# Kernel tuning notes

Measured on AMD Instinct MI355X. Metric: run time of the kernel, lower is better.

## Reference

```python
import jax, jax.numpy as jnp
import numpy as np

BETA = 0.95
THRESH = 1.0
T = 25
MAXD = 11      # dilated_kernel_size: 250//25=10 -> bumped to odd 11
LP = 10        # left_pad = 250//25
B = 1024
SIGINIT = 5.0  # max_delay // 2, SIG is frozen at this value


@jax.custom_vjp
def atan_spike(u):
    # heaviside forward, atan surrogate gradient (snntorch surrogate.atan, alpha=2)
    return (u > 0).astype(u.dtype)

def _atan_fwd(u):
    return atan_spike(u), u

def _atan_bwd(u, g):
    return (g / (1.0 + (jnp.pi * u) ** 2),)

atan_spike.defvjp(_atan_fwd, _atan_bwd)


def dcls_kernel(W, P, SIG):
    # DCLS 'gauss': gaussian-interpolated dense kernel.
    # W: (O, I, kc), P/SIG: (1, O, I, kc) -> dense kernel (O, I, MAXD)
    idx = jnp.arange(MAXD, dtype=W.dtype)
    Pc = P[0] + MAXD // 2                      # center positions in dense kernel
    S = jnp.abs(SIG[0]) + 0.27                 # sigma floor (DCLS epsilon)
    X = jnp.exp(-0.5 * ((idx[:, None, None, None] - Pc) / S) ** 2)  # (K,O,I,kc)
    X = X / (X.sum(axis=0, keepdims=True) + 1e-7)
    return jnp.einsum('oic,joic->oij', W, X)


def dcls_conv(x, W, P, SIG, b):
    # x: (B, C_in, L) -> (B, C_out, L - MAXD + 1), VALID conv like padding=0
    k = dcls_kernel(W, P, SIG)
    y = jax.lax.conv_general_dilated(x, k, (1,), 'VALID',
                                     dimension_numbers=('NCH', 'OIH', 'NCH'))
    return y + b[None, :, None]


def batchnorm(x, gamma, beta, mean, var, eps=1e-5):
    # eval-mode BatchNorm1d over (B, C, L)
    inv = gamma / jnp.sqrt(var + eps)
    return (x - mean[None, :, None]) * inv[None, :, None] + beta[None, :, None]


def lif_scan(x):
    # snntorch Leaky, reset_mechanism='subtract'; x: (B, C, T) input currents
    xT = jnp.moveaxis(x, 2, 0)  # (T, B, C)

    def step(mem, xt):
        reset = jax.lax.stop_gradient(atan_spike(mem - THRESH))  # detached reset
        mem = BETA * mem + xt - reset * THRESH
        spk = atan_spike(mem - THRESH)
        return mem, (spk, mem)

    _, (spk, mem) = jax.lax.scan(step, jnp.zeros_like(xT[0]), xT)
    return spk, mem  # each (T, B, C)


def pad_left(x):
    return jnp.pad(x, ((0, 0), (0, 0), (LP, 0)))


def setup_inputs() -> dict:
    key = jax.random.key(0)
    ks = jax.random.split(key, 16)

    def w_init(k, o, i):
        return jax.random.normal(k, (o, i, 1), jnp.float32) / np.sqrt(i)

    inp = {
        'data': jax.random.normal(ks[0], (B, T, 140), jnp.float32),
        'W1': w_init(ks[1], 256, 140),
        'b1': jax.random.normal(ks[2], (256,), jnp.float32) * 0.01,
        'P1': jax.random.uniform(ks[3], (1, 256, 140, 1), jnp.float32, -SIGINIT, SIGINIT),
        'SIG1': jnp.full((1, 256, 140, 1), SIGINIT, jnp.float32),
        'bn1_gamma': jax.random.uniform(ks[4], (256,), jnp.float32, 0.5, 1.5),
        'bn1_beta': jax.random.normal(ks[5], (256,), jnp.float32) * 0.1,
        'bn1_mean': jax.random.normal(ks[6], (256,), jnp.float32) * 0.1,
        'bn1_var': jax.random.uniform(ks[7], (256,), jnp.float32, 0.5, 1.5),
        'W2': w_init(ks[8], 256, 256),
        'b2': jax.random.normal(ks[9], (256,), jnp.float32) * 0.01,
        'P2': jax.random.uniform(ks[10], (1, 256, 256, 1), jnp.float32, -SIGINIT, SIGINIT),
        'SIG2': jnp.full((1, 256, 256, 1), SIGINIT, jnp.float32),
        'bn2_gamma': jax.random.uniform(ks[11], (256,), jnp.float32, 0.5, 1.5),
        'bn2_beta': jax.random.normal(ks[12], (256,), jnp.float32) * 0.1,
        'bn2_mean': jax.random.normal(ks[13], (256,), jnp.float32) * 0.1,
        'bn2_var': jax.random.uniform(ks[14], (256,), jnp.float32, 0.5, 1.5),
        'W3': w_init(ks[15], 20, 256),
        'b3': jnp.zeros((20,), jnp.float32),
        'P3': jax.random.uniform(jax.random.fold_in(key, 99), (1, 20, 256, 1), jnp.float32, -SIGINIT, SIGINIT),
        'SIG3': jnp.full((1, 20, 256, 1), SIGINIT, jnp.float32),
    }
    return inp


def reference(data, W1, b1, P1, SIG1, bn1_gamma, bn1_beta, bn1_mean, bn1_var,
              W2, b2, P2, SIG2, bn2_gamma, bn2_beta, bn2_mean, bn2_var,
              W3, b3, P3, SIG3):
    # data: (B, T, 140); pad time dim on the left, then to (B, C, L)
    x = jnp.moveaxis(jnp.pad(data, ((0, 0), (LP, 0), (0, 0))), 1, 2)  # (B,140,T+LP)
    x = batchnorm(dcls_conv(x, W1, P1, SIG1, b1), bn1_gamma, bn1_beta, bn1_mean, bn1_var)
    spk1, _ = lif_scan(x)                  # (T, B, 256)
    in1 = jnp.moveaxis(spk1, 0, 2)         # (B, 256, T)  (dropout eval = identity)

    x = batchnorm(dcls_conv(pad_left(in1), W2, P2, SIG2, b2),
                  bn2_gamma, bn2_beta, bn2_mean, bn2_var)
    spk2, _ = lif_scan(x)
    in2 = jnp.moveaxis(spk2, 0, 2)         # (B, 256, T)

    x = dcls_conv(pad_left(in2), W3, P3, SIG3, b3)  # (B, 20, T)
    spk3, mem3 = lif_scan(x)               # (T, B, 20) each
    return spk3, mem3
```

## Files before the change

### kernel.cpp

```cpp
#include <hip/hip_runtime.h>
#include <math.h>

#define BB 1024
#define TT 25
#define LP 10
#define MAXD 11

#define XR2 26
#define XC 264
#define XSZ2 (XR2 * XC)

#define IC1 140
#define ICP1 160
#define XC1 168
#define XSZ1 (XR2 * XC1)
#define SS1 (2 * XSZ1)

typedef __bf16 bf16x8 __attribute__((ext_vector_type(8)));
typedef float  f32x4  __attribute__((ext_vector_type(4)));

#define MFMA16(A, B, C) __builtin_amdgcn_mfma_f32_16x16x32_bf16((A), (B), (C), 0, 0, 0)

__global__ void gen_trip(const float* __restrict__ W,
                         const float* __restrict__ P,
                         const float* __restrict__ SIG,
                         __bf16* __restrict__ Khi, __bf16* __restrict__ Kmid,
                         __bf16* __restrict__ Klo,
                         int O, int Opad, int I, int Ipad) {
    int idx = blockIdx.x * blockDim.x + threadIdx.x;
    if (idx >= Opad * Ipad) return;
    int i = idx % Ipad;
    int o = idx / Ipad;
    if (o >= O || i >= I) {
#pragma unroll
        for (int j = 0; j < MAXD; ++j) {
            size_t ofs = ((size_t)(j * Opad + o)) * Ipad + i;
            Khi[ofs] = (__bf16)0.0f;
            Kmid[ofs] = (__bf16)0.0f;
            Klo[ofs] = (__bf16)0.0f;
        }
        return;
    }
    int widx = o * I + i;
    float w  = W[widx];
    float pc = P[widx] + (float)(MAXD / 2);
    float s  = fabsf(SIG[widx]) + 0.27f;
    float x[MAXD];
    float sum = 0.f;
#pragma unroll
    for (int j = 0; j < MAXD; ++j) {
        float d = ((float)j - pc) / s;
        x[j] = expf(-0.5f * d * d);
        sum += x[j];
    }
    float denom = sum + 1e-7f;
#pragma unroll
    for (int j = 0; j < MAXD; ++j) {
        float kv = w * (x[j] / denom);
        __bf16 h = (__bf16)kv;
        float  r1 = kv - (float)h;
        __bf16 m = (__bf16)r1;
        float  r2 = r1 - (float)m;
        __bf16 l = (__bf16)r2;
        size_t ofs = ((size_t)(j * Opad + o)) * Ipad + i;
        Khi[ofs] = h;
        Kmid[ofs] = m;
        Klo[ofs] = l;
    }
}

__global__ __launch_bounds__(512, 2)
void conv1_mfma(const float* __restrict__ xin,
                const __bf16* __restrict__ Khi,
                const __bf16* __restrict__ Kmid,
                const __bf16* __restrict__ Klo,
                const float* __restrict__ bias,
                const float* __restrict__ gamma,
                const float* __restrict__ beta,
                const float* __restrict__ mean,
                const float* __restrict__ var,
                __bf16* __restrict__ spk1) {
    __shared__ __align__(16) char smem[3 * SS1 * 2];
    __bf16* xs = (__bf16*)smem;
    float*  ys = (float*)smem;

    const int rr = blockIdx.x & 7;
    const int gg = blockIdx.x >> 3;
    const int pp = 2 * (rr + 8 * (gg >> 1)) + (gg & 1);
    const int b0 = pp * 2;

    const int tid  = threadIdx.x;
    const int w    = tid >> 6;
    const int lane = tid & 63;
    const int lm   = lane & 15;
    const int quad = lane >> 4;

    {
        uint32_t* xz = (uint32_t*)smem;
        for (int k = tid; k < 3 * SS1 / 2; k += 512) xz[k] = 0u;
    }
    __syncthreads();
#pragma unroll
    for (int bl = 0; bl < 2; ++bl) {
        const float* src = xin + (size_t)(b0 + bl) * (TT * IC1);
        for (int k = tid; k < TT * IC1; k += 512) {
            int t = k / IC1;
            int i = k - t * IC1;
            float x  = src[k];
            __bf16 h = (__bf16)x;
            float r1 = x - (float)h;
            __bf16 m = (__bf16)r1;
            float r2 = r1 - (float)m;
            __bf16 l = (__bf16)r2;
            int ofs = bl * XSZ1 + t * XC1 + i;
            xs[0 * SS1 + ofs] = h;
            xs[1 * SS1 + ofs] = m;
            xs[2 * SS1 + ofs] = l;
        }
    }
    __syncthreads();

    f32x4 acc[2][4];
#pragma unroll
    for (int p = 0; p < 2; ++p)
#pragma unroll
        for (int nt = 0; nt < 4; ++nt) acc[p][nt] = (f32x4){0.f, 0.f, 0.f, 0.f};

    auto loadA = [&](int n, bf16x8* Ah, bf16x8* Am, bf16x8* Al) {
        n = (n > 54) ? 54 : n;
        const int j = n / 5;
        const int ic = n - 5 * j;
        const size_t base =
            (size_t)(j * 256 + w * 32 + lm) * ICP1 + ic * 32 + quad * 8;
#pragma unroll
        for (int p = 0; p < 2; ++p) {
            Ah[p] = *(const bf16x8*)(Khi  + base + p * 16 * ICP1);
            Am[p] = *(const bf16x8*)(Kmid + base + p * 16 * ICP1);
            Al[p] = *(const bf16x8*)(Klo  + base + p * 16 * ICP1);
        }
    };

    auto step = [&](int n, bf16x8* Ah, bf16x8* Am, bf16x8* Al) {
        const int j = n / 5;
        const int ic = n - 5 * j;
        int r0 = lm + j - 10;          r0 = ((unsigned)r0 < 25u) ? r0 : 25;
        int r1 = 16 + lm + j - 10;     r1 = ((unsigned)r1 < 25u) ? r1 : 25;
        const int col = ic * 32 + quad * 8;
#pragma unroll
        for (int bl = 0; bl < 2; ++bl) {
            bf16x8 Bh[2], Bm[2], Bl[2];
#pragma unroll
            for (int th = 0; th < 2; ++th) {
                const int row = th ? r1 : r0;
                const int ofs = bl * XSZ1 + row * XC1 + col;
                Bh[th] = *(const bf16x8*)&xs[0 * SS1 + ofs];
                Bm[th] = *(const bf16x8*)&xs[1 * SS1 + ofs];
                Bl[th] = *(const bf16x8*)&xs[2 * SS1 + ofs];
            }
#pragma unroll
            for (int p = 0; p < 2; ++p)
#pragma unroll
                for (int th = 0; th < 2; ++th)
                    acc[p][bl * 2 + th] = MFMA16(Ah[p], Bh[th], acc[p][bl * 2 + th]);
#pragma unroll
            for (int p = 0; p < 2; ++p)
#pragma unroll
                for (int th = 0; th < 2; ++th)
                    acc[p][bl * 2 + th] = MFMA16(Ah[p], Bm[th], acc[p][bl * 2 + th]);
#pragma unroll
            for (int p = 0; p < 2; ++p)
#pragma unroll
                for (int th = 0; th < 2; ++th)
                    acc[p][bl * 2 + th] = MFMA16(Am[p], Bh[th], acc[p][bl * 2 + th]);
#pragma unroll
            for (int p = 0; p < 2; ++p)
#pragma unroll
                for (int th = 0; th < 2; ++th)
                    acc[p][bl * 2 + th] = MFMA16(Ah[p], Bl[th], acc[p][bl * 2 + th]);
#pragma unroll
            for (int p = 0; p < 2; ++p)
#pragma unroll
                for (int th = 0; th < 2; ++th)
                    acc[p][bl * 2 + th] = MFMA16(Am[p], Bm[th], acc[p][bl * 2 + th]);
#pragma unroll
            for (int p = 0; p < 2; ++p)
#pragma unroll
                for (int th = 0; th < 2; ++th)
                    acc[p][bl * 2 + th] = MFMA16(Al[p], Bh[th], acc[p][bl * 2 + th]);
        }
    };

    bf16x8 A0h[2], A0m[2], A0l[2], A1h[2], A1m[2], A1l[2];
    loadA(0, A0h, A0m, A0l);
    for (int n = 0; n < 54; n += 2) {
        loadA(n + 1, A1h, A1m, A1l);
        step(n, A0h, A0m, A0l);
        loadA(n + 2, A0h, A0m, A0l);
        step(n + 1, A1h, A1m, A1l);
    }
    step(54, A0h, A0m, A0l);

#pragma unroll
    for (int bl = 0; bl < 2; ++bl) {
        __syncthreads();
#pragma unroll
        for (int p = 0; p < 2; ++p)
#pragma unroll
            for (int th = 0; th < 2; ++th) {
                int t = th * 16 + lm;
                if (t < TT) {
                    int ob = w * 32 + p * 16 + quad * 4;
#pragma unroll
                    for (int v = 0; v < 4; ++v)
                        ys[(ob + v) * 27 + t] = acc[p][bl * 2 + th][v];
                }
            }
        __syncthreads();
        if (tid < 256) {
            const int o = tid;
            float scale = gamma[o] / sqrtf(var[o] + 1e-5f);
            float ofs   = (bias[o] - mean[o]) * scale + beta[o];
            unsigned short* dst =
                (unsigned short*)spk1 + (size_t)(b0 + bl) * (TT * 256) + o;
            const float* yrow = &ys[o * 27];
            float memv = 0.f;
#pragma unroll
            for (int t = 0; t < TT; ++t) {
                float a     = yrow[t] * scale + ofs;
                float reset = (memv > 1.0f) ? 1.0f : 0.f;
                memv        = 0.95f * memv + a - reset;
                dst[t * 256] = (memv > 1.0f) ? 0x3F80 : 0;
            }
        }
    }
}

__global__ __launch_bounds__(1024, 1)
void conv23_mfma(const __bf16* __restrict__ spk1,
                 const __bf16* __restrict__ Khi,
                 const __bf16* __restrict__ Kmid,
                 const __bf16* __restrict__ Klo,
                 const float* __restrict__ bias,
                 const float* __restrict__ gamma,
                 const float* __restrict__ beta,
                 const float* __restrict__ mean,
                 const float* __restrict__ var,
                 const __bf16* __restrict__ K3hi,
                 const __bf16* __restrict__ K3mid,
                 const __bf16* __restrict__ K3lo,
                 const float* __restrict__ b3,
                 float* __restrict__ out) {
    __shared__ __align__(16) char smem[61568];
    __bf16* xs  = (__bf16*)smem;
    float*  ysq = (float*)(smem + 54912);
    float*  ys3 = (float*)smem;

    const int b0   = blockIdx.x * 4;
    const int tid  = threadIdx.x;
    const int w    = tid >> 6;
    const int lane = tid & 63;
    const int lm   = lane & 15;
    const int quad = lane >> 4;

    for (int k = tid; k < 4 * (XC / 2); k += 1024) {
        int bl = k / (XC / 2);
        int c  = k % (XC / 2);
        ((uint32_t*)xs)[(bl * XSZ2 + 25 * XC) / 2 + c] = 0u;
    }
    for (int k = tid; k < 4 * 800; k += 1024) {
        int bl = k / 800;
        int v  = k % 800;
        int t  = v >> 5;
        int iv = v & 31;
        uint4 d = ((const uint4*)(spk1 + (size_t)(b0 + bl) * (TT * 256)))[v];
        *(uint4*)&xs[bl * XSZ2 + t * XC + iv * 8] = d;
    }
    __syncthreads();

    f32x4 acc[8];
#pragma unroll
    for (int nt = 0; nt < 8; ++nt) acc[nt] = (f32x4){0.f, 0.f, 0.f, 0.f};

    {
        auto loadA = [&](int n, bf16x8* Ah, bf16x8* Am, bf16x8* Al) {
            n = (n > 87) ? 87 : n;
            const int j = n >> 3, ic = n & 7;
            const size_t base =
                (size_t)(j * 256 + w * 16 + lm) * 256 + ic * 32 + quad * 8;
            *Ah = *(const bf16x8*)(Khi  + base);
            *Am = *(const bf16x8*)(Kmid + base);
            *Al = *(const bf16x8*)(Klo  + base);
        };
        auto step = [&](int n, bf16x8 Ah, bf16x8 Am, bf16x8 Al) {
            const int j = n >> 3, ic = n & 7;
            int r0 = lm + j - 10;          r0 = ((unsigned)r0 < 25u) ? r0 : 25;
            int r1 = 16 + lm + j - 10;     r1 = ((unsigned)r1 < 25u) ? r1 : 25;
            const int col = ic * 32 + quad * 8;
            bf16x8 Bf[8];
#pragma unroll
            for (int bl = 0; bl < 4; ++bl) {
                Bf[bl * 2 + 0] = *(const bf16x8*)&xs[bl * XSZ2 + r0 * XC + col];
                Bf[bl * 2 + 1] = *(const bf16x8*)&xs[bl * XSZ2 + r1 * XC + col];
            }
#pragma unroll
            for (int nt = 0; nt < 8; ++nt) acc[nt] = MFMA16(Ah, Bf[nt], acc[nt]);
#pragma unroll
            for (int nt = 0; nt < 8; ++nt) acc[nt] = MFMA16(Am, Bf[nt], acc[nt]);
#pragma unroll
            for (int nt = 0; nt < 8; ++nt) acc[nt] = MFMA16(Al, Bf[nt], acc[nt]);
        };

        bf16x8 A0h, A0m, A0l, A1h, A1m, A1l;
        loadA(0, &A0h, &A0m, &A0l);
        for (int n = 0; n < 86; n += 2) {
            loadA(n + 1, &A1h, &A1m, &A1l);
            step(n, A0h, A0m, A0l);
            loadA(n + 2, &A0h, &A0m, &A0l);
            step(n + 1, A1h, A1m, A1l);
        }
        loadA(87, &A1h, &A1m, &A1l);
        step(86, A0h, A0m, A0l);
        step(87, A1h, A1m, A1l);
    }

#pragma unroll
    for (int bl = 0; bl < 4; ++bl) {
#pragma unroll
        for (int q = 0; q < 4; ++q) {
            __syncthreads();
            if ((w >> 2) == q) {
#pragma unroll
                for (int th = 0; th < 2; ++th) {
                    int t = th * 16 + lm;
                    if (t < TT) {
                        int ol = (w & 3) * 16 + quad * 4;
#pragma unroll
                        for (int v = 0; v < 4; ++v)
                            ysq[(ol + v) * 26 + t] = acc[bl * 2 + th][v];
                    }
                }
            }
            __syncthreads();
            if (tid < 64) {
                const int o = q * 64 + tid;
                float scale = gamma[o] / sqrtf(var[o] + 1e-5f);
                float ofs   = (bias[o] - mean[o]) * scale + beta[o];
                const float* yrow = &ysq[tid * 26];
                unsigned short* sx = (unsigned short*)xs;
                float memv = 0.f;
#pragma unroll
                for (int t = 0; t < TT; ++t) {
                    float a     = yrow[t] * scale + ofs;
                    float reset = (memv > 1.0f) ? 1.0f : 0.f;
                    memv        = 0.95f * memv + a - reset;
                    sx[bl * XSZ2 + t * XC + o] = (memv > 1.0f) ? 0x3F80 : 0;
                }
            }
        }
    }
    __syncthreads();

    {
        const int p3  = w >> 3;
        const int bl3 = (w >> 1) & 3;
        const int th3 = w & 1;
        f32x4 accH, accM, accL;
        accH = (f32x4){0.f, 0.f, 0.f, 0.f};
        accM = (f32x4){0.f, 0.f, 0.f, 0.f};
        accL = (f32x4){0.f, 0.f, 0.f, 0.f};

        auto loadA3 = [&](int n, bf16x8* Ah, bf16x8* Am, bf16x8* Al) {
            n = (n > 87) ? 87 : n;
            const int j = n >> 3, ic = n & 7;
            const size_t kofs =
                ((size_t)(j * 32 + p3 * 16 + lm)) * 256 + ic * 32 + quad * 8;
            *Ah = *(const bf16x8*)(K3hi  + kofs);
            *Am = *(const bf16x8*)(K3mid + kofs);
            *Al = *(const bf16x8*)(K3lo  + kofs);
        };
        auto step3 = [&](int n, bf16x8 Ah, bf16x8 Am, bf16x8 Al) {
            const int j = n >> 3, ic = n & 7;
            int r = th3 * 16 + lm + j - 10;
            r = ((unsigned)r < 25u) ? r : 25;
            bf16x8 Bf =
                *(const bf16x8*)&xs[bl3 * XSZ2 + r * XC + ic * 32 + quad * 8];
            accH = MFMA16(Ah, Bf, accH);
            accM = MFMA16(Am, Bf, accM);
            accL = MFMA16(Al, Bf, accL);
        };

        bf16x8 A0h, A0m, A0l, A1h, A1m, A1l;
        loadA3(0, &A0h, &A0m, &A0l);
        for (int n = 0; n < 86; n += 2) {
            loadA3(n + 1, &A1h, &A1m, &A1l);
            step3(n, A0h, A0m, A0l);
            loadA3(n + 2, &A0h, &A0m, &A0l);
            step3(n + 1, A1h, A1m, A1l);
        }
        loadA3(87, &A1h, &A1m, &A1l);
        step3(86, A0h, A0m, A0l);
        step3(87, A1h, A1m, A1l);

        __syncthreads();
        {
            int t = th3 * 16 + lm;
            if (t < TT) {
#pragma unroll
                for (int v = 0; v < 4; ++v)
                    ys3[(bl3 * 32 + p3 * 16 + quad * 4 + v) * 26 + t] =
                        accH[v] + accM[v] + accL[v];
            }
        }
        __syncthreads();

        if (tid < 80) {
            const int bl2 = tid / 20;
            const int o   = tid % 20;
            float memv = 0.f;
            float bo   = b3[o];
            const float* yrow = &ys3[(bl2 * 32 + o) * 26];
#pragma unroll
            for (int t = 0; t < TT; ++t) {
                float a     = yrow[t] + bo;
                float reset = (memv > 1.0f) ? 1.0f : 0.f;
                memv        = 0.95f * memv + a - reset;
                float spk   = (memv > 1.0f) ? 1.0f : 0.f;
                out[(t * BB + (b0 + bl2)) * 20 + o]               = spk;
                out[TT * BB * 20 + (t * BB + (b0 + bl2)) * 20 + o] = memv;
            }
        }
    }
}

extern "C" void kernel_launch(void* const* d_in, const int* in_sizes, int n_in,
                              void* d_out, int out_size, void* d_ws, size_t ws_size,
                              hipStream_t stream) {
    const float* data = (const float*)d_in[0];
    const float* W1   = (const float*)d_in[1];
    const float* b1   = (const float*)d_in[2];
    const float* P1   = (const float*)d_in[3];
    const float* SIG1 = (const float*)d_in[4];
    const float* g1   = (const float*)d_in[5];
    const float* be1  = (const float*)d_in[6];
    const float* m1   = (const float*)d_in[7];
    const float* v1   = (const float*)d_in[8];
    const float* W2   = (const float*)d_in[9];
    const float* b2   = (const float*)d_in[10];
    const float* P2   = (const float*)d_in[11];
    const float* SIG2 = (const float*)d_in[12];
    const float* g2   = (const float*)d_in[13];
    const float* be2  = (const float*)d_in[14];
    const float* m2   = (const float*)d_in[15];
    const float* v2   = (const float*)d_in[16];
    const float* W3   = (const float*)d_in[17];
    const float* b3   = (const float*)d_in[18];
    const float* P3   = (const float*)d_in[19];
    const float* SIG3 = (const float*)d_in[20];
    float* out = (float*)d_out;

    char* p = (char*)d_ws;
    __bf16* K1hi  = (__bf16*)p;  p += 901120;
    __bf16* K1mid = (__bf16*)p;  p += 901120;
    __bf16* K1lo  = (__bf16*)p;  p += 901120;
    __bf16* spk1  = (__bf16*)p;  p += 13107200;
    __bf16* K2hi  = (__bf16*)p;  p += 1441792;
    __bf16* K2mid = (__bf16*)p;  p += 1441792;
    __bf16* K2lo  = (__bf16*)p;  p += 1441792;
    __bf16* K3hi  = (__bf16*)p;  p += 180224;
    __bf16* K3mid = (__bf16*)p;  p += 180224;
    __bf16* K3lo  = (__bf16*)p;

    gen_trip<<<(256 * 160 + 255) / 256, 256, 0, stream>>>(
        W1, P1, SIG1, K1hi, K1mid, K1lo, 256, 256, 140, 160);
    gen_trip<<<(256 * 256 + 255) / 256, 256, 0, stream>>>(
        W2, P2, SIG2, K2hi, K2mid, K2lo, 256, 256, 256, 256);
    gen_trip<<<(32 * 256 + 255) / 256, 256, 0, stream>>>(
        W3, P3, SIG3, K3hi, K3mid, K3lo, 20, 32, 256, 256);

    conv1_mfma<<<BB / 2, 512, 0, stream>>>(data, K1hi, K1mid, K1lo,
                                           b1, g1, be1, m1, v1, spk1);
    conv23_mfma<<<BB / 4, 1024, 0, stream>>>(spk1, K2hi, K2mid, K2lo,
                                             b2, g2, be2, m2, v2,
                                             K3hi, K3mid, K3lo, b3, out);
}
```

Baseline: 473.5 us.

## Halve conv23 batch per block and give each wave two output tiles

The conv23 kernel now handles 2 batch samples per 512-thread block instead of 4 per 1024-thread block. This doubles the grid to 512 blocks and roughly halves LDS use, so more blocks can be resident per CU. Each wave now computes two 16-row output-channel tiles, loading twice the A fragments while reusing each B fragment across both tiles. The conv1 block-index swizzle is also dropped in favour of linear batch mapping. In exchange, every K2 weight fragment is fetched from global memory by twice as many blocks, and each wave needs more registers.

```diff
diff --git a/kernel.cpp b/kernel.cpp
--- a/kernel.cpp
+++ b/kernel.cpp
@@ -84,10 +84,7 @@
     __bf16* xs = (__bf16*)smem;
     float*  ys = (float*)smem;
 
-    const int rr = blockIdx.x & 7;
-    const int gg = blockIdx.x >> 3;
-    const int pp = 2 * (rr + 8 * (gg >> 1)) + (gg & 1);
-    const int b0 = pp * 2;
+    const int b0 = blockIdx.x * 2;
 
     const int tid  = threadIdx.x;
     const int w    = tid >> 6;
@@ -235,7 +232,7 @@
     }
 }
 
-__global__ __launch_bounds__(1024, 1)
+__global__ __launch_bounds__(512, 4)
 void conv23_mfma(const __bf16* __restrict__ spk1,
                  const __bf16* __restrict__ Khi,
                  const __bf16* __restrict__ Kmid,
@@ -250,24 +247,24 @@
                  const __bf16* __restrict__ K3lo,
                  const float* __restrict__ b3,
                  float* __restrict__ out) {
-    __shared__ __align__(16) char smem[61568];
+    __shared__ __align__(16) char smem[34112];
     __bf16* xs  = (__bf16*)smem;
-    float*  ysq = (float*)(smem + 54912);
+    float*  ysq = (float*)(smem + 27456);
     float*  ys3 = (float*)smem;
 
-    const int b0   = blockIdx.x * 4;
+    const int b0   = blockIdx.x * 2;
     const int tid  = threadIdx.x;
     const int w    = tid >> 6;
     const int lane = tid & 63;
     const int lm   = lane & 15;
     const int quad = lane >> 4;
 
-    for (int k = tid; k < 4 * (XC / 2); k += 1024) {
+    for (int k = tid; k < 2 * (XC / 2); k += 512) {
         int bl = k / (XC / 2);
         int c  = k % (XC / 2);
         ((uint32_t*)xs)[(bl * XSZ2 + 25 * XC) / 2 + c] = 0u;
     }
-    for (int k = tid; k < 4 * 800; k += 1024) {
+    for (int k = tid; k < 2 * 800; k += 512) {
         int bl = k / 800;
         int v  = k % 800;
         int t  = v >> 5;
@@ -277,68 +274,84 @@
     }
     __syncthreads();
 
-    f32x4 acc[8];
-#pragma unroll
-    for (int nt = 0; nt < 8; ++nt) acc[nt] = (f32x4){0.f, 0.f, 0.f, 0.f};
+    f32x4 acc[2][4];
+#pragma unroll
+    for (int pi = 0; pi < 2; ++pi)
+#pragma unroll
+        for (int nt = 0; nt < 4; ++nt) acc[pi][nt] = (f32x4){0.f, 0.f, 0.f, 0.f};
 
     {
         auto loadA = [&](int n, bf16x8* Ah, bf16x8* Am, bf16x8* Al) {
             n = (n > 87) ? 87 : n;
             const int j = n >> 3, ic = n & 7;
-            const size_t base =
-                (size_t)(j * 256 + w * 16 + lm) * 256 + ic * 32 + quad * 8;
-            *Ah = *(const bf16x8*)(Khi  + base);
-            *Am = *(const bf16x8*)(Kmid + base);
-            *Al = *(const bf16x8*)(Klo  + base);
+#pragma unroll
+            for (int pi = 0; pi < 2; ++pi) {
+                const size_t base =
+                    (size_t)(j * 256 + w * 32 + pi * 16 + lm) * 256 + ic * 32 + quad * 8;
+                Ah[pi] = *(const bf16x8*)(Khi  + base);
+                Am[pi] = *(const bf16x8*)(Kmid + base);
+                Al[pi] = *(const bf16x8*)(Klo  + base);
+            }
         };
-        auto step = [&](int n, bf16x8 Ah, bf16x8 Am, bf16x8 Al) {
+        auto step = [&](int n, bf16x8* Ah, bf16x8* Am, bf16x8* Al) {
             const int j = n >> 3, ic = n & 7;
             int r0 = lm + j - 10;          r0 = ((unsigned)r0 < 25u) ? r0 : 25;
             int r1 = 16 + lm + j - 10;     r1 = ((unsigned)r1 < 25u) ? r1 : 25;
             const int col = ic * 32 + quad * 8;
-            bf16x8 Bf[8];
-#pragma unroll
-            for (int bl = 0; bl < 4; ++bl) {
+            bf16x8 Bf[4];
+#pragma unroll
+            for (int bl = 0; bl < 2; ++bl) {
                 Bf[bl * 2 + 0] = *(const bf16x8*)&xs[bl * XSZ2 + r0 * XC + col];
                 Bf[bl * 2 + 1] = *(const bf16x8*)&xs[bl * XSZ2 + r1 * XC + col];
             }
 #pragma unroll
-            for (int nt = 0; nt < 8; ++nt) acc[nt] = MFMA16(Ah, Bf[nt], acc[nt]);
-#pragma unroll
-            for (int nt = 0; nt < 8; ++nt) acc[nt] = MFMA16(Am, Bf[nt], acc[nt]);
-#pragma unroll
-            for (int nt = 0; nt < 8; ++nt) acc[nt] = MFMA16(Al, Bf[nt], acc[nt]);
+            for (int pi = 0; pi < 2; ++pi)
+#pragma unroll
+                for (int nt = 0; nt < 4; ++nt)
+                    acc[pi][nt] = MFMA16(Ah[pi], Bf[nt], acc[pi][nt]);
+#pragma unroll
+            for (int pi = 0; pi < 2; ++pi)
+#pragma unroll
+                for (int nt = 0; nt < 4; ++nt)
+                    acc[pi][nt] = MFMA16(Am[pi], Bf[nt], acc[pi][nt]);
+#pragma unroll
+            for (int pi = 0; pi < 2; ++pi)
+#pragma unroll
+                for (int nt = 0; nt < 4; ++nt)
+                    acc[pi][nt] = MFMA16(Al[pi], Bf[nt], acc[pi][nt]);
         };
 
-        bf16x8 A0h, A0m, A0l, A1h, A1m, A1l;
-        loadA(0, &A0h, &A0m, &A0l);
+        bf16x8 A0h[2], A0m[2], A0l[2], A1h[2], A1m[2], A1l[2];
+        loadA(0, A0h, A0m, A0l);
         for (int n = 0; n < 86; n += 2) {
-            loadA(n + 1, &A1h, &A1m, &A1l);
+            loadA(n + 1, A1h, A1m, A1l);
             step(n, A0h, A0m, A0l);
-            loadA(n + 2, &A0h, &A0m, &A0l);
+            loadA(n + 2, A0h, A0m, A0l);
             step(n + 1, A1h, A1m, A1l);
         }
-        loadA(87, &A1h, &A1m, &A1l);
+        loadA(87, A1h, A1m, A1l);
         step(86, A0h, A0m, A0l);
         step(87, A1h, A1m, A1l);
     }
 
 #pragma unroll
-    for (int bl = 0; bl < 4; ++bl) {
+    for (int bl = 0; bl < 2; ++bl) {
 #pragma unroll
         for (int q = 0; q < 4; ++q) {
             __syncthreads();
-            if ((w >> 2) == q) {
-#pragma unroll
-                for (int th = 0; th < 2; ++th) {
-                    int t = th * 16 + lm;
-                    if (t < TT) {
-                        int ol = (w & 3) * 16 + quad * 4;
-#pragma unroll
-                        for (int v = 0; v < 4; ++v)
-                            ysq[(ol + v) * 26 + t] = acc[bl * 2 + th][v];
+            if ((w >> 1) == q) {
+#pragma unroll
+                for (int pi = 0; pi < 2; ++pi)
+#pragma unroll
+                    for (int th = 0; th < 2; ++th) {
+                        int t = th * 16 + lm;
+                        if (t < TT) {
+                            int ol = (w & 1) * 32 + pi * 16 + quad * 4;
+#pragma unroll
+                            for (int v = 0; v < 4; ++v)
+                                ysq[(ol + v) * 26 + t] = acc[pi][bl * 2 + th][v];
+                        }
                     }
-                }
             }
             __syncthreads();
             if (tid < 64) {
@@ -361,8 +374,8 @@
     __syncthreads();
 
     {
-        const int p3  = w >> 3;
-        const int bl3 = (w >> 1) & 3;
+        const int p3  = w >> 2;
+        const int bl3 = (w >> 1) & 1;
         const int th3 = w & 1;
         f32x4 accH, accM, accL;
         accH = (f32x4){0.f, 0.f, 0.f, 0.f};
@@ -413,7 +426,7 @@
         }
         __syncthreads();
 
-        if (tid < 80) {
+        if (tid < 40) {
             const int bl2 = tid / 20;
             const int o   = tid % 20;
             float memv = 0.f;
@@ -479,7 +492,7 @@
 
     conv1_mfma<<<BB / 2, 512, 0, stream>>>(data, K1hi, K1mid, K1lo,
                                            b1, g1, be1, m1, v1, spk1);
-    conv23_mfma<<<BB / 4, 1024, 0, stream>>>(spk1, K2hi, K2mid, K2lo,
-                                             b2, g2, be2, m2, v2,
-                                             K3hi, K3mid, K3lo, b3, out);
+    conv23_mfma<<<BB / 2, 512, 0, stream>>>(spk1, K2hi, K2mid, K2lo,
+                                            b2, g2, be2, m2, v2,
+                                            K3hi, K3mid, K3lo, b3, out);
 }
```

New measurement: 577.8 us. +22.0%, slower.
